# Kernel optimization log

Measured on AMD Instinct MI355X. Metric: run time of the kernel, lower is better.

Reference implementation:

```python
import jax, jax.numpy as jnp
import numpy as np

D = 256      # d_model
H = 8        # n_heads
L = 4        # n_levels
P = 4        # n_points
DFF = 1024   # d_ffn
DH = D // H  # head dim
SPATIAL = np.array([[100, 100], [50, 50], [25, 25], [13, 13]], dtype=np.int64)  # (H_l, W_l)
LV = int((SPATIAL[:, 0] * SPATIAL[:, 1]).sum())  # 13294 flattened memory tokens


def layer_norm(x, w, b, eps=1e-5):
    m = jnp.mean(x, -1, keepdims=True)
    v = jnp.mean((x - m) ** 2, -1, keepdims=True)
    return (x - m) * jax.lax.rsqrt(v + eps) * w + b


def setup_inputs() -> dict:
    key = jax.random.key(0)
    ks = jax.random.split(key, 16)
    nq, bs = 900, 8

    def w(k, shape, s=0.02):
        return jax.random.normal(k, shape, dtype=jnp.float32) * s

    return {
        "tgt": jax.random.normal(ks[0], (nq, bs, D), jnp.float32),
        "tgt_query_pos": jax.random.normal(ks[1], (nq, bs, D), jnp.float32),
        "tgt_reference_points": jax.random.uniform(ks[2], (nq, bs, L, 2), jnp.float32),
        "memory": jax.random.normal(ks[3], (LV, bs, D), jnp.float32),
        "sa_Wqkv": w(ks[4], (3 * D, D)), "sa_bqkv": jnp.zeros((3 * D,), jnp.float32),
        "sa_Wo": w(ks[5], (D, D)), "sa_bo": jnp.zeros((D,), jnp.float32),
        "ln1_w": jnp.ones((D,), jnp.float32), "ln1_b": jnp.zeros((D,), jnp.float32),
        "ln2_w": jnp.ones((D,), jnp.float32), "ln2_b": jnp.zeros((D,), jnp.float32),
        "ln3_w": jnp.ones((D,), jnp.float32), "ln3_b": jnp.zeros((D,), jnp.float32),
        "ca_Woff": w(ks[6], (H * L * P * 2, D)), "ca_boff": w(ks[7], (H * L * P * 2,), 0.5),
        "ca_Wattn": w(ks[8], (H * L * P, D)), "ca_battn": jnp.zeros((H * L * P,), jnp.float32),
        "ca_Wval": w(ks[9], (D, D)), "ca_bval": jnp.zeros((D,), jnp.float32),
        "ca_Wout": w(ks[10], (D, D)), "ca_bout": jnp.zeros((D,), jnp.float32),
        "ffn_W1": w(ks[11], (DFF, D)), "ffn_b1": jnp.zeros((DFF,), jnp.float32),
        "ffn_W2": w(ks[12], (D, DFF)), "ffn_b2": jnp.zeros((D,), jnp.float32),
        "memory_key_padding_mask": jnp.zeros((bs, LV), jnp.bool_),
        "memory_spatial_shapes": jnp.asarray(SPATIAL),
    }


def msdeform_attn(query, ref, value, mask, shapes_np,
                  Woff, boff, Wattn, battn, Wval, bval, Wout, bout):
    # query: [bs,nq,D], ref: [bs,nq,L,2], value: [bs,lv,D], mask: [bs,lv]
    bs, nq, _ = query.shape
    lv = value.shape[1]
    v = value @ Wval.T + bval
    v = jnp.where(mask[:, :, None], 0.0, v)
    v = v.reshape(bs, lv, H, DH).transpose(0, 2, 1, 3)  # [bs,H,lv,DH]
    off = (query @ Woff.T + boff).reshape(bs, nq, H, L, P, 2)
    aw = jax.nn.softmax((query @ Wattn.T + battn).reshape(bs, nq, H, L * P), -1)
    aw = aw.reshape(bs, nq, H, L, P)
    # offset normalizer is [W_l, H_l]
    norm = jnp.asarray(shapes_np[:, ::-1].copy(), jnp.float32)  # [L,2]
    loc = ref[:, :, None, :, None, :] + off / norm[None, None, None, :, None, :]
    out = jnp.zeros((bs, nq, H, DH), jnp.float32)
    start = 0
    for l in range(L):
        Hl, Wl = int(shapes_np[l, 0]), int(shapes_np[l, 1])
        vf = v[:, :, start:start + Hl * Wl]  # [bs,H,Hl*Wl,DH]
        start += Hl * Wl
        # grid_sample(align_corners=False) pixel coords
        x = loc[:, :, :, l, :, 0] * Wl - 0.5  # [bs,nq,H,P]
        y = loc[:, :, :, l, :, 1] * Hl - 0.5
        x0 = jnp.floor(x); y0 = jnp.floor(y)
        fx = x - x0; fy = y - y0
        x0i = x0.astype(jnp.int32); y0i = y0.astype(jnp.int32)

        def gather(yi, xi):
            valid = ((xi >= 0) & (xi < Wl) & (yi >= 0) & (yi < Hl)).astype(jnp.float32)
            idx = jnp.clip(yi, 0, Hl - 1) * Wl + jnp.clip(xi, 0, Wl - 1)
            idx_t = idx.transpose(0, 2, 1, 3).reshape(bs, H, nq * P, 1)
            g = jnp.take_along_axis(vf, idx_t, axis=2)  # [bs,H,nq*P,DH]
            return g * valid.transpose(0, 2, 1, 3).reshape(bs, H, nq * P, 1)

        def wgt(w):
            return w.transpose(0, 2, 1, 3).reshape(bs, H, nq * P, 1)

        samp = (gather(y0i, x0i) * wgt((1 - fx) * (1 - fy))
                + gather(y0i, x0i + 1) * wgt(fx * (1 - fy))
                + gather(y0i + 1, x0i) * wgt((1 - fx) * fy)
                + gather(y0i + 1, x0i + 1) * wgt(fx * fy))
        samp = samp.reshape(bs, H, nq, P, DH)
        out = out + jnp.einsum('bhqpd,bqhp->bqhd', samp, aw[:, :, :, l])
    return out.reshape(bs, nq, D) @ Wout.T + bout


def reference(tgt, tgt_query_pos, tgt_reference_points, memory,
              sa_Wqkv, sa_bqkv, sa_Wo, sa_bo,
              ln1_w, ln1_b, ln2_w, ln2_b, ln3_w, ln3_b,
              ca_Woff, ca_boff, ca_Wattn, ca_battn, ca_Wval, ca_bval, ca_Wout, ca_bout,
              ffn_W1, ffn_b1, ffn_W2, ffn_b2,
              memory_key_padding_mask, memory_spatial_shapes):
    shapes_np = np.asarray(memory_spatial_shapes)  # static per trace
    nq, bs, _ = tgt.shape
    # --- self attention (post-LN, residual) ---
    q = tgt + tgt_query_pos
    qp = (q @ sa_Wqkv[:D].T + sa_bqkv[:D]).reshape(nq, bs, H, DH)
    kp = (q @ sa_Wqkv[D:2 * D].T + sa_bqkv[D:2 * D]).reshape(nq, bs, H, DH)
    vp = (tgt @ sa_Wqkv[2 * D:].T + sa_bqkv[2 * D:]).reshape(nq, bs, H, DH)
    scores = jnp.einsum('qbhd,kbhd->bhqk', qp, kp) * (1.0 / float(np.sqrt(DH)))
    attn = jax.nn.softmax(scores, -1)
    o = jnp.einsum('bhqk,kbhd->qbhd', attn, vp).reshape(nq, bs, D) @ sa_Wo.T + sa_bo
    tgt = layer_norm(tgt + o, ln2_w, ln2_b)
    # --- multi-scale deformable cross attention ---
    query = (tgt + tgt_query_pos).transpose(1, 0, 2)      # [bs,nq,D]
    ref = tgt_reference_points.transpose(1, 0, 2, 3)      # [bs,nq,L,2]
    val = memory.transpose(1, 0, 2)                       # [bs,lv,D]
    ca = msdeform_attn(query, ref, val, memory_key_padding_mask, shapes_np,
                       ca_Woff, ca_boff, ca_Wattn, ca_battn,
                       ca_Wval, ca_bval, ca_Wout, ca_bout).transpose(1, 0, 2)
    tgt = layer_norm(tgt + ca, ln1_w, ln1_b)
    # --- FFN ---
    t2 = jax.nn.relu(tgt @ ffn_W1.T + ffn_b1) @ ffn_W2.T + ffn_b2
    return layer_norm(tgt + t2, ln3_w, ln3_b)
```

## Files before the change

### kernel.cpp

```cpp
#include <hip/hip_runtime.h>
#include <hip/hip_bf16.h>

#define NQ   900
#define BSZ  8
#define DM   256
#define NH   8
#define DHD  32
#define DFF_ 1024
#define LVTOT 13294
#define NTOK (NQ*BSZ)
#define MVAL (LVTOT*BSZ)

typedef __attribute__((ext_vector_type(8))) short bf16x8;
typedef __attribute__((ext_vector_type(4))) short bf16x4;
typedef __attribute__((ext_vector_type(4))) float f32x4;
typedef unsigned int u32;

__device__ __forceinline__ unsigned short f2bf(float x) {
  union { __hip_bfloat16 h; unsigned short u; } cv;
  cv.h = __float2bfloat16(x);
  return cv.u;
}
__device__ __forceinline__ float bf2f(unsigned short u) {
  union { __hip_bfloat16 h; unsigned short u; } cv;
  cv.u = u;
  return __bfloat162float(cv.h);
}

__device__ __forceinline__ void gl_lds16(const void* gsrc, void* ldst) {
  __builtin_amdgcn_global_load_lds(
      (const __attribute__((address_space(1))) u32*)gsrc,
      (__attribute__((address_space(3))) u32*)ldst, 16, 0, 0);
}

__global__ __launch_bounds__(256) void addcast_kernel(const float* __restrict__ a,
                                                      const float* __restrict__ b,
                                                      unsigned short* __restrict__ o, int n8) {
  int i = blockIdx.x * 256 + threadIdx.x;
  if (i >= n8) return;
  float4 a0 = ((const float4*)a)[i * 2], a1 = ((const float4*)a)[i * 2 + 1];
  float4 b0 = ((const float4*)b)[i * 2], b1 = ((const float4*)b)[i * 2 + 1];
  bf16x8 v;
  v[0] = (short)f2bf(a0.x + b0.x); v[1] = (short)f2bf(a0.y + b0.y);
  v[2] = (short)f2bf(a0.z + b0.z); v[3] = (short)f2bf(a0.w + b0.w);
  v[4] = (short)f2bf(a1.x + b1.x); v[5] = (short)f2bf(a1.y + b1.y);
  v[6] = (short)f2bf(a1.z + b1.z); v[7] = (short)f2bf(a1.w + b1.w);
  *(bf16x8*)(o + (long)i * 8) = v;
}

__global__ __launch_bounds__(256) void cast_weights_kernel(
    const float* p0, const float* p1, const float* p2, const float* p3,
    const float* p4, const float* p5, const float* p6, const float* p7,
    unsigned short* dst) {
  long i8 = ((long)blockIdx.x * 256 + threadIdx.x) * 8;
  if (i8 >= 1015808) return;
  const float* src; long off;
  if      (i8 < 196608) { src = p0; off = i8; }
  else if (i8 < 262144) { src = p1; off = i8 - 196608; }
  else if (i8 < 327680) { src = p2; off = i8 - 262144; }
  else if (i8 < 393216) { src = p3; off = i8 - 327680; }
  else if (i8 < 425984) { src = p4; off = i8 - 393216; }
  else if (i8 < 491520) { src = p5; off = i8 - 425984; }
  else if (i8 < 753664) { src = p6; off = i8 - 491520; }
  else                  { src = p7; off = i8 - 753664; }
  float4 a = *(const float4*)(src + off);
  float4 b = *(const float4*)(src + off + 4);
  bf16x8 v;
  v[0] = (short)f2bf(a.x); v[1] = (short)f2bf(a.y);
  v[2] = (short)f2bf(a.z); v[3] = (short)f2bf(a.w);
  v[4] = (short)f2bf(b.x); v[5] = (short)f2bf(b.y);
  v[6] = (short)f2bf(b.z); v[7] = (short)f2bf(b.w);
  *(bf16x8*)(dst + i8) = v;
}

__global__ __launch_bounds__(256) void concat_bias_kernel(const float* __restrict__ a,
                                                          const float* __restrict__ b,
                                                          float* __restrict__ o) {
  int i = blockIdx.x * 256 + threadIdx.x;
  if (i < 256) o[i] = a[i];
  else if (i < 384) o[i] = b[i - 256];
}

template <int AF32, int OUT_BF16, int RELU>
__global__ __launch_bounds__(256) void gemm_mfma_kernel(
    const void* __restrict__ Araw, const unsigned short* __restrict__ W,
    const float* __restrict__ bias, void* __restrict__ C,
    int M, int K, int ldc) {
  constexpr int ABYTES = AF32 ? 16384 : 8192;
  __shared__ alignas(16) unsigned char As0[ABYTES];
  __shared__ alignas(16) unsigned char As1[ABYTES];
  __shared__ alignas(16) unsigned char Bs0[8192];
  __shared__ alignas(16) unsigned char Bs1[8192];
  int tid = threadIdx.x;
  int l = tid & 63, w = tid >> 6;
  int lr = l & 15, lg = l >> 4;
  int wr = w >> 1, wc = w & 1;
  int n0 = blockIdx.x * 128, m0 = blockIdx.y * 128;

  f32x4 acc[4][4];
#pragma unroll
  for (int m = 0; m < 4; m++)
#pragma unroll
    for (int n = 0; n < 4; n++) acc[m][n] = (f32x4){0.f, 0.f, 0.f, 0.f};

  auto stage = [&](unsigned char* Ab, unsigned char* Bb, int k0) {
#pragma unroll
    for (int i = 0; i < 2; i++) {
      int c16 = i * 4 + w;
      int row = c16 * 16 + (l >> 2);
      int sc = (l & 3) ^ (row & 3);
      gl_lds16(W + (long)(n0 + row) * K + k0 + sc * 8, Bb + c16 * 1024 + l * 16);
    }
    if (AF32) {
      const float* Af = (const float*)Araw;
#pragma unroll
      for (int i = 0; i < 4; i++) {
        int c8 = i * 4 + w;
        int row = c8 * 8 + (l >> 3);
        int g = m0 + row; if (g >= M) g = M - 1;
        int sc = (l & 7) ^ (row & 7);
        gl_lds16(Af + (long)g * K + k0 + sc * 4, Ab + c8 * 1024 + l * 16);
      }
    } else {
      const unsigned short* A = (const unsigned short*)Araw;
#pragma unroll
      for (int i = 0; i < 2; i++) {
        int c16 = i * 4 + w;
        int row = c16 * 16 + (l >> 2);
        int g = m0 + row; if (g >= M) g = M - 1;
        int sc = (l & 3) ^ (row & 3);
        gl_lds16(A + (long)g * K + k0 + sc * 8, Ab + c16 * 1024 + l * 16);
      }
    }
  };

  auto compute = [&](const unsigned char* Ab, const unsigned char* Bb) {
    bf16x8 af[4], bfr[4];
    if (AF32) {
#pragma unroll
      for (int m = 0; m < 4; m++) {
        int row = wr * 64 + m * 16 + lr;
        f32x4 fa = *(const f32x4*)(Ab + row * 128 + (((lg * 2)     ^ (lr & 7)) * 16));
        f32x4 fb = *(const f32x4*)(Ab + row * 128 + (((lg * 2 + 1) ^ (lr & 7)) * 16));
        bf16x8 v;
        v[0] = (short)f2bf(fa[0]); v[1] = (short)f2bf(fa[1]);
        v[2] = (short)f2bf(fa[2]); v[3] = (short)f2bf(fa[3]);
        v[4] = (short)f2bf(fb[0]); v[5] = (short)f2bf(fb[1]);
        v[6] = (short)f2bf(fb[2]); v[7] = (short)f2bf(fb[3]);
        af[m] = v;
      }
    } else {
#pragma unroll
      for (int m = 0; m < 4; m++) {
        int row = wr * 64 + m * 16 + lr;
        af[m] = *(const bf16x8*)(Ab + row * 64 + ((lg ^ (lr & 3)) * 16));
      }
    }
#pragma unroll
    for (int n = 0; n < 4; n++) {
      int row = wc * 64 + n * 16 + lr;
      bfr[n] = *(const bf16x8*)(Bb + row * 64 + ((lg ^ (lr & 3)) * 16));
    }
#pragma unroll
    for (int m = 0; m < 4; m++)
#pragma unroll
      for (int n = 0; n < 4; n++)
        acc[m][n] = __builtin_amdgcn_mfma_f32_16x16x32_bf16(af[m], bfr[n], acc[m][n], 0, 0, 0);
  };

  int nt = K >> 5;
  stage(As0, Bs0, 0);
  for (int t = 0; t < nt; t += 2) {
    __syncthreads();
    stage(As1, Bs1, (t + 1) << 5);
    __builtin_amdgcn_sched_barrier(0);
    compute(As0, Bs0);
    __syncthreads();
    if (t + 2 < nt) stage(As0, Bs0, (t + 2) << 5);
    __builtin_amdgcn_sched_barrier(0);
    compute(As1, Bs1);
  }

  float bv[4];
#pragma unroll
  for (int ni = 0; ni < 4; ni++) bv[ni] = bias[n0 + wc * 64 + ni * 16 + lr];
#pragma unroll
  for (int mi = 0; mi < 4; mi++) {
#pragma unroll
    for (int r = 0; r < 4; r++) {
      int row = m0 + wr * 64 + mi * 16 + lg * 4 + r;
      if (row < M) {
#pragma unroll
        for (int ni = 0; ni < 4; ni++) {
          int col = n0 + wc * 64 + ni * 16 + lr;
          float v = acc[mi][ni][r] + bv[ni];
          if (RELU) v = fmaxf(v, 0.f);
          if (OUT_BF16) ((unsigned short*)C)[(long)row * ldc + col] = f2bf(v);
          else          ((float*)C)[(long)row * ldc + col] = v;
        }
      }
    }
  }
}

__global__ __launch_bounds__(256) void attn_mfma_kernel(const unsigned short* __restrict__ qkv,
                                                        unsigned short* __restrict__ out) {
  __shared__ unsigned short Vt[32][72];
  __shared__ unsigned short Ps[4][16][72];
  int tid = threadIdx.x;
  int l = tid & 63, w = tid >> 6;
  int lr = l & 15, lg = l >> 4;
  int q0 = blockIdx.x * 64;
  int h = blockIdx.y & 7, b = blockIdx.y >> 3;
  const float scale = 0.17677669529663687f;

  int qrow = q0 + w * 16 + lr;
  int qclamp = qrow < 899 ? qrow : 899;
  bf16x8 qf = *(const bf16x8*)(qkv + ((long)qclamp * 8 + b) * 768 + h * 32 + lg * 8);

  f32x4 o_acc[2];
  o_acc[0] = (f32x4){0.f, 0.f, 0.f, 0.f};
  o_acc[1] = (f32x4){0.f, 0.f, 0.f, 0.f};
  float m_run[4] = {-1e30f, -1e30f, -1e30f, -1e30f};
  float l_run[4] = {0.f, 0.f, 0.f, 0.f};

  for (int k0 = 0; k0 < NQ; k0 += 64) {
    __syncthreads();
    {
      int key = tid >> 2, dg = tid & 3;
      int kk = k0 + key; if (kk > 899) kk = 899;
      bf16x8 vv = *(const bf16x8*)(qkv + ((long)kk * 8 + b) * 768 + 512 + h * 32 + dg * 8);
#pragma unroll
      for (int j = 0; j < 8; j++) Vt[dg * 8 + j][key] = (unsigned short)vv[j];
    }
    f32x4 sg[4];
#pragma unroll
    for (int ng = 0; ng < 4; ng++) {
      int key = k0 + ng * 16 + lr; int kc = key < 899 ? key : 899;
      bf16x8 kf = *(const bf16x8*)(qkv + ((long)kc * 8 + b) * 768 + 256 + h * 32 + lg * 8);
      sg[ng] = __builtin_amdgcn_mfma_f32_16x16x32_bf16(qf, kf, (f32x4){0.f, 0.f, 0.f, 0.f}, 0, 0, 0);
    }
    float sv[4][4];
#pragma unroll
    for (int ng = 0; ng < 4; ng++) {
      bool bad = (k0 + ng * 16 + lr) >= NQ;
#pragma unroll
      for (int r = 0; r < 4; r++) sv[ng][r] = bad ? -1e30f : sg[ng][r] * scale;
    }
    float p[4][4];
#pragma unroll
    for (int r = 0; r < 4; r++) {
      float rmax = fmaxf(fmaxf(sv[0][r], sv[1][r]), fmaxf(sv[2][r], sv[3][r]));
#pragma unroll
      for (int mk = 8; mk; mk >>= 1) rmax = fmaxf(rmax, __shfl_xor(rmax, mk));
      float mnew = fmaxf(m_run[r], rmax);
      float fs = __expf(m_run[r] - mnew);
      m_run[r] = mnew;
      float ps = 0.f;
#pragma unroll
      for (int ng = 0; ng < 4; ng++) { p[ng][r] = __expf(sv[ng][r] - mnew); ps += p[ng][r]; }
#pragma unroll
      for (int mk = 8; mk; mk >>= 1) ps += __shfl_xor(ps, mk);
      l_run[r] = l_run[r] * fs + ps;
      o_acc[0][r] *= fs;
      o_acc[1][r] *= fs;
    }
#pragma unroll
    for (int ng = 0; ng < 4; ng++)
#pragma unroll
      for (int r = 0; r < 4; r++)
        Ps[w][lg * 4 + r][lr + ng * 16] = f2bf(p[ng][r]);
    __syncthreads();
#pragma unroll
    for (int ks = 0; ks < 2; ks++) {
      bf16x8 pf = *(const bf16x8*)&Ps[w][lr][ks * 32 + lg * 8];
#pragma unroll
      for (int ni = 0; ni < 2; ni++) {
        bf16x8 vf = *(const bf16x8*)&Vt[ni * 16 + lr][ks * 32 + lg * 8];
        o_acc[ni] = __builtin_amdgcn_mfma_f32_16x16x32_bf16(pf, vf, o_acc[ni], 0, 0, 0);
      }
    }
  }
#pragma unroll
  for (int r = 0; r < 4; r++) {
    int orow = q0 + w * 16 + lg * 4 + r;
    if (orow < NQ) {
      float inv = 1.f / l_run[r];
      unsigned short* op = out + ((long)orow * 8 + b) * 256 + h * 32 + lr;
      op[0]  = f2bf(o_acc[0][r] * inv);
      op[16] = f2bf(o_acc[1][r] * inv);
    }
  }
}

__device__ __forceinline__ void fetch8_acc(const unsigned short* __restrict__ vtmp, int lo, int W,
                                           int yi, int xi, int b, int col0, float wgt,
                                           float* a) {
  if ((xi < 0) | (xi >= W) | (yi < 0) | (yi >= W)) return;
  const unsigned short* p = vtmp + ((long)((lo + yi * W + xi) * BSZ + b)) * 256 + col0;
  bf16x8 r = *(const bf16x8*)p;
#pragma unroll
  for (int j = 0; j < 8; j++) a[j] += wgt * bf2f((unsigned short)r[j]);
}

__global__ __launch_bounds__(256) void sampler_kernel(const unsigned short* __restrict__ vtmp,
                                                      const float* __restrict__ oa,
                                                      const float* __restrict__ ref,
                                                      unsigned short* __restrict__ samp) {
  __shared__ float s_off[8][256];
  __shared__ float s_aw[8][128];
  __shared__ float s_ref[8][8];
  int tid = threadIdx.x;
  int t0 = blockIdx.x * 8;
#pragma unroll
  for (int k = 0; k < 8; k++) s_off[k][tid] = oa[(long)(t0 + k) * 384 + tid];
#pragma unroll
  for (int i = 0; i < 4; i++) {
    int idx = i * 256 + tid;
    int k = idx >> 7, c = idx & 127;
    s_aw[k][c] = oa[(long)(t0 + k) * 384 + 256 + c];
  }
  if (tid < 64) s_ref[tid >> 3][tid & 7] = ref[(long)(t0 + (tid >> 3)) * 8 + (tid & 7)];
  __syncthreads();
  if (tid < 64) {
    int k = tid >> 3, hh = tid & 7;
    float* p = &s_aw[k][hh * 16];
    float m = -1e30f;
#pragma unroll
    for (int j = 0; j < 16; j++) m = fmaxf(m, p[j]);
    float s = 0.f;
#pragma unroll
    for (int j = 0; j < 16; j++) { p[j] = __expf(p[j] - m); s += p[j]; }
    float inv = 1.f / s;
#pragma unroll
    for (int j = 0; j < 16; j++) p[j] *= inv;
  }
  __syncthreads();
  int w = tid >> 5;
  int l = tid & 31;
  int t = t0 + w;
  int h = l >> 2, col0 = h * 32 + (l & 3) * 8;
  int b = t & 7;
  const int Wls[4]  = {100, 50, 25, 13};
  const int lofs[4] = {0, 10000, 12500, 13125};
  float a[8];
#pragma unroll
  for (int j = 0; j < 8; j++) a[j] = 0.f;
#pragma unroll
  for (int lvl = 0; lvl < 4; lvl++) {
    int W = Wls[lvl];
    float Wf = (float)W;
    int lo = lofs[lvl];
    float rx = s_ref[w][lvl * 2 + 0], ry = s_ref[w][lvl * 2 + 1];
#pragma unroll
    for (int p = 0; p < 4; p++) {
      float ox = s_off[w][((h * 4 + lvl) * 4 + p) * 2 + 0];
      float oy = s_off[w][((h * 4 + lvl) * 4 + p) * 2 + 1];
      float x = rx * Wf + ox - 0.5f;
      float y = ry * Wf + oy - 0.5f;
      float x0f = floorf(x), y0f = floorf(y);
      float fx = x - x0f, fy = y - y0f;
      int x0 = (int)x0f, y0 = (int)y0f;
      float aa = s_aw[w][h * 16 + lvl * 4 + p];
      float w00 = aa * (1.f - fx) * (1.f - fy);
      float w01 = aa * fx * (1.f - fy);
      float w10 = aa * (1.f - fx) * fy;
      float w11 = aa * fx * fy;
      fetch8_acc(vtmp, lo, W, y0,     x0,     b, col0, w00, a);
      fetch8_acc(vtmp, lo, W, y0,     x0 + 1, b, col0, w01, a);
      fetch8_acc(vtmp, lo, W, y0 + 1, x0,     b, col0, w10, a);
      fetch8_acc(vtmp, lo, W, y0 + 1, x0 + 1, b, col0, w11, a);
    }
  }
  bf16x8 o;
#pragma unroll
  for (int j = 0; j < 8; j++) o[j] = (short)f2bf(a[j]);
  *(bf16x8*)(samp + (long)t * 256 + col0) = o;
}

__global__ __launch_bounds__(256) void ln_kernel(const float* __restrict__ x,
                                                 const float* __restrict__ res,
                                                 const float* __restrict__ w,
                                                 const float* __restrict__ bvec,
                                                 float* __restrict__ out,
                                                 unsigned short* __restrict__ out_bf,
                                                 const float* __restrict__ pos,
                                                 unsigned short* __restrict__ pos_bf,
                                                 int rows) {
  int wv = threadIdx.x >> 6, lane = threadIdx.x & 63;
  int row = blockIdx.x * 4 + wv;
  if (row >= rows) return;
  float4 xv = *(const float4*)(x + (long)row * 256 + lane * 4);
  float4 rv = *(const float4*)(res + (long)row * 256 + lane * 4);
  float v0 = xv.x + rv.x, v1 = xv.y + rv.y, v2 = xv.z + rv.z, v3 = xv.w + rv.w;
  float s = v0 + v1 + v2 + v3;
#pragma unroll
  for (int o = 32; o; o >>= 1) s += __shfl_xor(s, o);
  float mean = s * (1.f / 256.f);
  float d0 = v0 - mean, d1 = v1 - mean, d2 = v2 - mean, d3 = v3 - mean;
  float q = d0 * d0 + d1 * d1 + d2 * d2 + d3 * d3;
#pragma unroll
  for (int o = 32; o; o >>= 1) q += __shfl_xor(q, o);
  float rstd = rsqrtf(q * (1.f / 256.f) + 1e-5f);
  float4 wv4 = *(const float4*)(w + lane * 4);
  float4 bv4 = *(const float4*)(bvec + lane * 4);
  float o0 = d0 * rstd * wv4.x + bv4.x;
  float o1 = d1 * rstd * wv4.y + bv4.y;
  float o2 = d2 * rstd * wv4.z + bv4.z;
  float o3 = d3 * rstd * wv4.w + bv4.w;
  *(float4*)(out + (long)row * 256 + lane * 4) = make_float4(o0, o1, o2, o3);
  if (out_bf) {
    unsigned short* p = out_bf + (long)row * 256 + lane * 4;
    p[0] = f2bf(o0); p[1] = f2bf(o1); p[2] = f2bf(o2); p[3] = f2bf(o3);
  }
  if (pos_bf) {
    float4 pv = *(const float4*)(pos + (long)row * 256 + lane * 4);
    unsigned short* p = pos_bf + (long)row * 256 + lane * 4;
    p[0] = f2bf(o0 + pv.x); p[1] = f2bf(o1 + pv.y);
    p[2] = f2bf(o2 + pv.z); p[3] = f2bf(o3 + pv.w);
  }
}

extern "C" void kernel_launch(void* const* d_in, const int* in_sizes, int n_in,
                              void* d_out, int out_size, void* d_ws, size_t ws_size,
                              hipStream_t stream) {
  const float* tgt     = (const float*)d_in[0];
  const float* pos     = (const float*)d_in[1];
  const float* refpts  = (const float*)d_in[2];
  const float* memory  = (const float*)d_in[3];
  const float* sa_Wqkv = (const float*)d_in[4];
  const float* sa_bqkv = (const float*)d_in[5];
  const float* sa_Wo   = (const float*)d_in[6];
  const float* sa_bo   = (const float*)d_in[7];
  const float* ln1_w   = (const float*)d_in[8];
  const float* ln1_b   = (const float*)d_in[9];
  const float* ln2_w   = (const float*)d_in[10];
  const float* ln2_b   = (const float*)d_in[11];
  const float* ln3_w   = (const float*)d_in[12];
  const float* ln3_b   = (const float*)d_in[13];
  const float* ca_Woff = (const float*)d_in[14];
  const float* ca_boff = (const float*)d_in[15];
  const float* ca_Wattn= (const float*)d_in[16];
  const float* ca_battn= (const float*)d_in[17];
  const float* ca_Wval = (const float*)d_in[18];
  const float* ca_bval = (const float*)d_in[19];
  const float* ca_Wout = (const float*)d_in[20];
  const float* ca_bout = (const float*)d_in[21];
  const float* ffn_W1  = (const float*)d_in[22];
  const float* ffn_b1  = (const float*)d_in[23];
  const float* ffn_W2  = (const float*)d_in[24];
  const float* ffn_b2  = (const float*)d_in[25];

  char* ws = (char*)d_ws;
  float*          buf_ca = (float*)(ws);
  float*          buf_t3 = (float*)(ws + 8388608);
  unsigned short* t3_bf  = (unsigned short*)(ws + 16777216);
  unsigned short* buf_h  = (unsigned short*)(ws + 20971520);
  float*          buf_f  = (float*)(ws + 36700160);
  float*          bias_cat = (float*)(ws + 44072960);
  unsigned short* buf_v  = (unsigned short*)(ws + 54452224);
  unsigned short* wts    = (unsigned short*)(ws + 112590848);
  unsigned short* buf_q  = (unsigned short*)(ws + 114622464);
  unsigned short* buf_qkv= (unsigned short*)(ws + 118308864);
  float*          buf_oa = (float*)(ws + 118308864);
  unsigned short* buf_o  = (unsigned short*)(ws + 129368064);
  unsigned short* buf_smp= (unsigned short*)(ws + 129368064);
  float*          buf_t2 = (float*)(ws + 133054464);

  const unsigned short* w_qkv = wts + 0;
  const unsigned short* w_o   = wts + 196608;
  const unsigned short* w_val = wts + 262144;
  const unsigned short* w_oa  = wts + 327680;
  const unsigned short* w_out = wts + 425984;
  const unsigned short* w_f1  = wts + 491520;
  const unsigned short* w_f2  = wts + 753664;

  dim3 blk(256);
  const int n8tok = NTOK * DM / 8;

  cast_weights_kernel<<<(1015808 / 8 + 255) / 256, blk, 0, stream>>>(
      sa_Wqkv, sa_Wo, ca_Wval, ca_Woff, ca_Wattn, ca_Wout, ffn_W1, ffn_W2, wts);
  concat_bias_kernel<<<2, blk, 0, stream>>>(ca_boff, ca_battn, bias_cat);
  addcast_kernel<<<(n8tok + 255) / 256, blk, 0, stream>>>(tgt, pos, buf_q, n8tok);
  gemm_mfma_kernel<0, 1, 0><<<dim3(4, 57), blk, 0, stream>>>(buf_q, w_qkv, sa_bqkv,
                                                             buf_qkv, NTOK, 256, 768);
  gemm_mfma_kernel<1, 1, 0><<<dim3(2, 57), blk, 0, stream>>>(tgt, w_qkv + 512 * 256,
                                                             sa_bqkv + 512, buf_qkv + 512,
                                                             NTOK, 256, 768);
  gemm_mfma_kernel<1, 1, 0><<<dim3(2, 831), blk, 0, stream>>>(memory, w_val, ca_bval,
                                                              buf_v, MVAL, 256, 256);
  attn_mfma_kernel<<<dim3(15, 64), blk, 0, stream>>>(buf_qkv, buf_o);
  gemm_mfma_kernel<0, 0, 0><<<dim3(2, 57), blk, 0, stream>>>(buf_o, w_o, sa_bo,
                                                             buf_t2, NTOK, 256, 256);
  ln_kernel<<<1800, blk, 0, stream>>>(buf_t2, tgt, ln2_w, ln2_b, buf_t2, nullptr,
                                      pos, buf_q, NTOK);
  gemm_mfma_kernel<0, 0, 0><<<dim3(3, 57), blk, 0, stream>>>(buf_q, w_oa, bias_cat,
                                                             buf_oa, NTOK, 256, 384);
  sampler_kernel<<<NTOK / 8, blk, 0, stream>>>(buf_v, buf_oa, refpts, buf_smp);
  gemm_mfma_kernel<0, 0, 0><<<dim3(2, 57), blk, 0, stream>>>(buf_smp, w_out, ca_bout,
                                                             buf_ca, NTOK, 256, 256);
  ln_kernel<<<1800, blk, 0, stream>>>(buf_ca, buf_t2, ln1_w, ln1_b, buf_t3, t3_bf,
                                      nullptr, nullptr, NTOK);
  gemm_mfma_kernel<0, 1, 1><<<dim3(8, 57), blk, 0, stream>>>(t3_bf, w_f1, ffn_b1,
                                                             buf_h, NTOK, 256, 1024);
  gemm_mfma_kernel<0, 0, 0><<<dim3(2, 57), blk, 0, stream>>>(buf_h, w_f2, ffn_b2,
                                                             buf_f, NTOK, 1024, 256);
  ln_kernel<<<1800, blk, 0, stream>>>(buf_f, buf_t3, ln3_w, ln3_b, (float*)d_out, nullptr,
                                      nullptr, nullptr, NTOK);
}
```

Before: 233.3 us.

## Triple-buffer GEMM LDS staging with explicit vmcnt waits

Replaces the double-buffered K loop in the MFMA GEMM with a three-stage ring buffer that keeps two tiles of global-to-LDS loads in flight. Uses hand-counted s_waitcnt vmcnt values and raw s_barrier instead of __syncthreads, so only the oldest stage is waited on. The aim is to hide global load latency better, at the cost of extra LDS use (up to 72KB for the fp32-A variant), which lowers occupancy. The hard-coded vmcnt counts must match the number of loads issued per stage. Stages are also not issued for K tiles past the end, and the initial three stages assume K is at least 96.

After: 256.4 us. +9.9%, slower.

```diff
diff --git a/kernel.cpp b/kernel.cpp
--- a/kernel.cpp
+++ b/kernel.cpp
@@ -87,10 +87,9 @@
     const float* __restrict__ bias, void* __restrict__ C,
     int M, int K, int ldc) {
   constexpr int ABYTES = AF32 ? 16384 : 8192;
-  __shared__ alignas(16) unsigned char As0[ABYTES];
-  __shared__ alignas(16) unsigned char As1[ABYTES];
-  __shared__ alignas(16) unsigned char Bs0[8192];
-  __shared__ alignas(16) unsigned char Bs1[8192];
+  constexpr int LPT = AF32 ? 6 : 4;
+  __shared__ alignas(16) unsigned char As[3][ABYTES];
+  __shared__ alignas(16) unsigned char Bs[3][8192];
   int tid = threadIdx.x;
   int l = tid & 63, w = tid >> 6;
   int lr = l & 15, lg = l >> 4;
@@ -103,13 +102,13 @@
 #pragma unroll
     for (int n = 0; n < 4; n++) acc[m][n] = (f32x4){0.f, 0.f, 0.f, 0.f};
 
-  auto stage = [&](unsigned char* Ab, unsigned char* Bb, int k0) {
+  auto stage = [&](int buf, int k0) {
 #pragma unroll
     for (int i = 0; i < 2; i++) {
       int c16 = i * 4 + w;
       int row = c16 * 16 + (l >> 2);
       int sc = (l & 3) ^ (row & 3);
-      gl_lds16(W + (long)(n0 + row) * K + k0 + sc * 8, Bb + c16 * 1024 + l * 16);
+      gl_lds16(W + (long)(n0 + row) * K + k0 + sc * 8, Bs[buf] + c16 * 1024 + l * 16);
     }
     if (AF32) {
       const float* Af = (const float*)Araw;
@@ -119,7 +118,7 @@
         int row = c8 * 8 + (l >> 3);
         int g = m0 + row; if (g >= M) g = M - 1;
         int sc = (l & 7) ^ (row & 7);
-        gl_lds16(Af + (long)g * K + k0 + sc * 4, Ab + c8 * 1024 + l * 16);
+        gl_lds16(Af + (long)g * K + k0 + sc * 4, As[buf] + c8 * 1024 + l * 16);
       }
     } else {
       const unsigned short* A = (const unsigned short*)Araw;
@@ -129,19 +128,19 @@
         int row = c16 * 16 + (l >> 2);
         int g = m0 + row; if (g >= M) g = M - 1;
         int sc = (l & 3) ^ (row & 3);
-        gl_lds16(A + (long)g * K + k0 + sc * 8, Ab + c16 * 1024 + l * 16);
+        gl_lds16(A + (long)g * K + k0 + sc * 8, As[buf] + c16 * 1024 + l * 16);
       }
     }
   };
 
-  auto compute = [&](const unsigned char* Ab, const unsigned char* Bb) {
+  auto compute = [&](int buf) {
     bf16x8 af[4], bfr[4];
     if (AF32) {
 #pragma unroll
       for (int m = 0; m < 4; m++) {
         int row = wr * 64 + m * 16 + lr;
-        f32x4 fa = *(const f32x4*)(Ab + row * 128 + (((lg * 2)     ^ (lr & 7)) * 16));
-        f32x4 fb = *(const f32x4*)(Ab + row * 128 + (((lg * 2 + 1) ^ (lr & 7)) * 16));
+        f32x4 fa = *(const f32x4*)(As[buf] + row * 128 + (((lg * 2)     ^ (lr & 7)) * 16));
+        f32x4 fb = *(const f32x4*)(As[buf] + row * 128 + (((lg * 2 + 1) ^ (lr & 7)) * 16));
         bf16x8 v;
         v[0] = (short)f2bf(fa[0]); v[1] = (short)f2bf(fa[1]);
         v[2] = (short)f2bf(fa[2]); v[3] = (short)f2bf(fa[3]);
@@ -153,13 +152,13 @@
 #pragma unroll
       for (int m = 0; m < 4; m++) {
         int row = wr * 64 + m * 16 + lr;
-        af[m] = *(const bf16x8*)(Ab + row * 64 + ((lg ^ (lr & 3)) * 16));
+        af[m] = *(const bf16x8*)(As[buf] + row * 64 + ((lg ^ (lr & 3)) * 16));
       }
     }
 #pragma unroll
     for (int n = 0; n < 4; n++) {
       int row = wc * 64 + n * 16 + lr;
-      bfr[n] = *(const bf16x8*)(Bb + row * 64 + ((lg ^ (lr & 3)) * 16));
+      bfr[n] = *(const bf16x8*)(Bs[buf] + row * 64 + ((lg ^ (lr & 3)) * 16));
     }
 #pragma unroll
     for (int m = 0; m < 4; m++)
@@ -169,16 +168,27 @@
   };
 
   int nt = K >> 5;
-  stage(As0, Bs0, 0);
-  for (int t = 0; t < nt; t += 2) {
-    __syncthreads();
-    stage(As1, Bs1, (t + 1) << 5);
+  stage(0, 0);
+  stage(1, 32);
+  stage(2, 64);
+
+  for (int t = 0; t < nt; t++) {
+    int ahead = nt - 1 - t;
+    if (ahead >= 2) {
+      if (AF32) asm volatile("s_waitcnt vmcnt(12)" ::: "memory");
+      else      asm volatile("s_waitcnt vmcnt(8)"  ::: "memory");
+    } else if (ahead == 1) {
+      if (AF32) asm volatile("s_waitcnt vmcnt(6)" ::: "memory");
+      else      asm volatile("s_waitcnt vmcnt(4)" ::: "memory");
+    } else {
+      asm volatile("s_waitcnt vmcnt(0)" ::: "memory");
+    }
+    __builtin_amdgcn_s_barrier();
     __builtin_amdgcn_sched_barrier(0);
-    compute(As0, Bs0);
-    __syncthreads();
-    if (t + 2 < nt) stage(As0, Bs0, (t + 2) << 5);
+    compute(t % 3);
     __builtin_amdgcn_sched_barrier(0);
-    compute(As1, Bs1);
+    __builtin_amdgcn_s_barrier();
+    if (t + 3 < nt) stage(t % 3, (t + 3) << 5);
   }
 
   float bv[4];
```

## Triple-buffer GEMM K-loop with vmcnt-based waits and compile-time K

Applied to the files above, without the earlier changes.

Replaces the double-buffered GEMM main loop with a three-stage LDS ring that prefetches two tiles ahead. It uses explicit s_waitcnt vmcnt counts and raw s_barrier in place of __syncthreads, and makes K a template parameter so the loop fully unrolls. The aim is to hide global-load latency behind MFMA work in these short-K GEMMs. In exchange LDS per block grows by half, which can lower occupancy (especially for the fp32-A variant), and the hand-tuned vmcnt values depend on the exact number of loads per stage.

Measured after the change: 234.9 us. Within noise of the previous version (+0.7%).

```diff
diff --git a/kernel.cpp b/kernel.cpp
--- a/kernel.cpp
+++ b/kernel.cpp
@@ -81,16 +81,19 @@
   else if (i < 384) o[i] = b[i - 256];
 }
 
-template <int AF32, int OUT_BF16, int RELU>
+template <int AF32, int OUT_BF16, int RELU, int NT>
 __global__ __launch_bounds__(256) void gemm_mfma_kernel(
     const void* __restrict__ Araw, const unsigned short* __restrict__ W,
     const float* __restrict__ bias, void* __restrict__ C,
-    int M, int K, int ldc) {
+    int M, int ldc) {
+  constexpr int K = NT * 32;
   constexpr int ABYTES = AF32 ? 16384 : 8192;
   __shared__ alignas(16) unsigned char As0[ABYTES];
   __shared__ alignas(16) unsigned char As1[ABYTES];
+  __shared__ alignas(16) unsigned char As2[ABYTES];
   __shared__ alignas(16) unsigned char Bs0[8192];
   __shared__ alignas(16) unsigned char Bs1[8192];
+  __shared__ alignas(16) unsigned char Bs2[8192];
   int tid = threadIdx.x;
   int l = tid & 63, w = tid >> 6;
   int lr = l & 15, lg = l >> 4;
@@ -168,17 +171,31 @@
         acc[m][n] = __builtin_amdgcn_mfma_f32_16x16x32_bf16(af[m], bfr[n], acc[m][n], 0, 0, 0);
   };
 
-  int nt = K >> 5;
+  unsigned char* Abuf[3] = {As0, As1, As2};
+  unsigned char* Bbuf[3] = {Bs0, Bs1, Bs2};
   stage(As0, Bs0, 0);
-  for (int t = 0; t < nt; t += 2) {
-    __syncthreads();
-    stage(As1, Bs1, (t + 1) << 5);
+  stage(As1, Bs1, 32);
+  stage(As2, Bs2, 64);
+
+#pragma unroll
+  for (int t = 0; t < NT; t++) {
+    const int ahead = NT - 1 - t;
+    if (ahead >= 2) {
+      if (AF32) asm volatile("s_waitcnt vmcnt(12)" ::: "memory");
+      else      asm volatile("s_waitcnt vmcnt(8)"  ::: "memory");
+    } else if (ahead == 1) {
+      if (AF32) asm volatile("s_waitcnt vmcnt(6)" ::: "memory");
+      else      asm volatile("s_waitcnt vmcnt(4)" ::: "memory");
+    } else {
+      asm volatile("s_waitcnt vmcnt(0)" ::: "memory");
+    }
+    __builtin_amdgcn_s_barrier();
     __builtin_amdgcn_sched_barrier(0);
-    compute(As0, Bs0);
-    __syncthreads();
-    if (t + 2 < nt) stage(As0, Bs0, (t + 2) << 5);
+    compute(Abuf[t % 3], Bbuf[t % 3]);
     __builtin_amdgcn_sched_barrier(0);
-    compute(As1, Bs1);
+    __builtin_amdgcn_s_barrier();
+    __builtin_amdgcn_sched_barrier(0);
+    if (t + 3 < NT) stage(Abuf[t % 3], Bbuf[t % 3], (t + 3) * 32);
   }
 
   float bv[4];
@@ -482,29 +499,29 @@
       sa_Wqkv, sa_Wo, ca_Wval, ca_Woff, ca_Wattn, ca_Wout, ffn_W1, ffn_W2, wts);
   concat_bias_kernel<<<2, blk, 0, stream>>>(ca_boff, ca_battn, bias_cat);
   addcast_kernel<<<(n8tok + 255) / 256, blk, 0, stream>>>(tgt, pos, buf_q, n8tok);
-  gemm_mfma_kernel<0, 1, 0><<<dim3(4, 57), blk, 0, stream>>>(buf_q, w_qkv, sa_bqkv,
-                                                             buf_qkv, NTOK, 256, 768);
-  gemm_mfma_kernel<1, 1, 0><<<dim3(2, 57), blk, 0, stream>>>(tgt, w_qkv + 512 * 256,
-                                                             sa_bqkv + 512, buf_qkv + 512,
-                                                             NTOK, 256, 768);
-  gemm_mfma_kernel<1, 1, 0><<<dim3(2, 831), blk, 0, stream>>>(memory, w_val, ca_bval,
-                                                              buf_v, MVAL, 256, 256);
+  gemm_mfma_kernel<0, 1, 0, 8><<<dim3(4, 57), blk, 0, stream>>>(buf_q, w_qkv, sa_bqkv,
+                                                                buf_qkv, NTOK, 768);
+  gemm_mfma_kernel<1, 1, 0, 8><<<dim3(2, 57), blk, 0, stream>>>(tgt, w_qkv + 512 * 256,
+                                                                sa_bqkv + 512, buf_qkv + 512,
+                                                                NTOK, 768);
+  gemm_mfma_kernel<1, 1, 0, 8><<<dim3(2, 831), blk, 0, stream>>>(memory, w_val, ca_bval,
+                                                                 buf_v, MVAL, 256);
   attn_mfma_kernel<<<dim3(15, 64), blk, 0, stream>>>(buf_qkv, buf_o);
-  gemm_mfma_kernel<0, 0, 0><<<dim3(2, 57), blk, 0, stream>>>(buf_o, w_o, sa_bo,
-                                                             buf_t2, NTOK, 256, 256);
+  gemm_mfma_kernel<0, 0, 0, 8><<<dim3(2, 57), blk, 0, stream>>>(buf_o, w_o, sa_bo,
+                                                                buf_t2, NTOK, 256);
   ln_kernel<<<1800, blk, 0, stream>>>(buf_t2, tgt, ln2_w, ln2_b, buf_t2, nullptr,
                                       pos, buf_q, NTOK);
-  gemm_mfma_kernel<0, 0, 0><<<dim3(3, 57), blk, 0, stream>>>(buf_q, w_oa, bias_cat,
-                                                             buf_oa, NTOK, 256, 384);
+  gemm_mfma_kernel<0, 0, 0, 8><<<dim3(3, 57), blk, 0, stream>>>(buf_q, w_oa, bias_cat,
+                                                                buf_oa, NTOK, 384);
   sampler_kernel<<<NTOK / 8, blk, 0, stream>>>(buf_v, buf_oa, refpts, buf_smp);
-  gemm_mfma_kernel<0, 0, 0><<<dim3(2, 57), blk, 0, stream>>>(buf_smp, w_out, ca_bout,
-                                                             buf_ca, NTOK, 256, 256);
+  gemm_mfma_kernel<0, 0, 0, 8><<<dim3(2, 57), blk, 0, stream>>>(buf_smp, w_out, ca_bout,
+                                                                buf_ca, NTOK, 256);
   ln_kernel<<<1800, blk, 0, stream>>>(buf_ca, buf_t2, ln1_w, ln1_b, buf_t3, t3_bf,
                                       nullptr, nullptr, NTOK);
-  gemm_mfma_kernel<0, 1, 1><<<dim3(8, 57), blk, 0, stream>>>(t3_bf, w_f1, ffn_b1,
-                                                             buf_h, NTOK, 256, 1024);
-  gemm_mfma_kernel<0, 0, 0><<<dim3(2, 57), blk, 0, stream>>>(buf_h, w_f2, ffn_b2,
-                                                             buf_f, NTOK, 1024, 256);
+  gemm_mfma_kernel<0, 1, 1, 8><<<dim3(8, 57), blk, 0, stream>>>(t3_bf, w_f1, ffn_b1,
+                                                                buf_h, NTOK, 1024);
+  gemm_mfma_kernel<0, 0, 0, 32><<<dim3(2, 57), blk, 0, stream>>>(buf_h, w_f2, ffn_b2,
+                                                                 buf_f, NTOK, 256);
   ln_kernel<<<1800, blk, 0, stream>>>(buf_f, buf_t3, ln3_w, ln3_b, (float*)d_out, nullptr,
                                       nullptr, nullptr, NTOK);
 }
```
